# Kernel optimization log

Measured on AMD Instinct MI355X. Metric: run time of the kernel, lower is better.

The kernel has to match this reference:

```python
import jax, jax.numpy as jnp
import numpy as np

N = 50000      # nodes
E = 800000     # edges (before self-loops)
IN = 64        # input feature dim
SLOPE = 0.2    # leaky_relu negative slope
# layer specs: (heads, out_channels, concat)
LAYERS = [(8, 8, True), (8, 8, True), (4, 1, False)]


def _glorot(key, shape):
    fan = shape[-2] + shape[-1]
    lim = np.sqrt(6.0 / fan).astype(np.float32)
    return jax.random.uniform(key, shape, jnp.float32, -lim, lim)


def setup_inputs() -> dict:
    key = jax.random.key(0)
    ks = jax.random.split(key, 12)
    X = jax.random.normal(ks[0], (N, IN), jnp.float32)
    src = jax.random.randint(ks[1], (E,), 0, N)
    dst = jax.random.randint(ks[2], (E,), 0, N)
    dst = jnp.where(dst == src, (dst + 1) % N, dst)  # no self-loops (module removes then re-adds them)
    edge_index = jnp.stack([src, dst]).astype(jnp.int64)
    inp = {"X": X, "edge_index": edge_index}
    in_c = IN
    for li, (H, C, concat) in enumerate(LAYERS):
        k1, k2 = jax.random.split(ks[3 + li], 2)
        inp[f"W{li+1}"] = _glorot(k1, (in_c, H * C))
        inp[f"att{li+1}"] = _glorot(k2, (1, H, 2 * C))
        inp[f"b{li+1}"] = jnp.zeros((H * C if concat else C,), jnp.float32)
        in_c = H * C
    return inp


def _gat_layer(x, src, dst, W, att, b, heads, C, concat):
    # linear projection then view as [N, H, C]
    xw = (x @ W).reshape(-1, heads, C)
    # attention logits decompose: (cat[x_i, x_j] * att).sum(-1) = a_i[dst] + a_j[src]
    a_i = jnp.einsum('nhc,hc->nh', xw, att[0, :, :C])   # target-side score per node
    a_j = jnp.einsum('nhc,hc->nh', xw, att[0, :, C:])   # source-side score per node
    e = a_i[dst] + a_j[src]                              # [E', H]
    e = jnp.where(e > 0, e, SLOPE * e)                   # leaky_relu
    # segment softmax over edges sharing the same target node (stable)
    emax = jax.ops.segment_max(e, dst, num_segments=N)
    ex = jnp.exp(e - emax[dst])
    denom = jax.ops.segment_sum(ex, dst, num_segments=N)
    alpha = ex / denom[dst]                              # [E', H]
    # weighted scatter-add of source messages
    out = jax.ops.segment_sum(xw[src] * alpha[:, :, None], dst, num_segments=N)  # [N, H, C]
    out = out.reshape(-1, heads * C) if concat else out.mean(axis=1)
    return out + b


def reference(X, edge_index, W1, att1, b1, W2, att2, b2, W3, att3, b3):
    # add self-loops (module removes any existing then adds one per node)
    loop = jnp.arange(N, dtype=edge_index.dtype)
    src = jnp.concatenate([edge_index[0], loop])
    dst = jnp.concatenate([edge_index[1], loop])
    params = [(W1, att1, b1), (W2, att2, b2), (W3, att3, b3)]
    x = X
    for li, ((H, C, concat), (W, att, b)) in enumerate(zip(LAYERS, params)):
        x = _gat_layer(x, src, dst, W, att, b, H, C, concat)
        if li + 1 < len(LAYERS):
            x = jax.nn.relu(x)
    return x  # [N, 1]
```

## Files before the change

kernel.cpp:

```cpp
#include <hip/hip_runtime.h>
#include <hip/hip_bf16.h>
#include <hip/hip_fp16.h>
#include <float.h>


#define FDIM 64
#define BSHIFT 7
#define BNODES (1 << BSHIFT)
#define BINCH 8192

__device__ __forceinline__ int clampN(int v, int N) {
  return ((unsigned)v >= (unsigned)N) ? 0 : v;
}

__global__ __launch_bounds__(256) void init_kernel(
    const int* __restrict__ ei, int E, int* __restrict__ bucketCount, int NB,
    int* __restrict__ flag) {
  int i = blockIdx.x * 256 + threadIdx.x;
  if (i < NB) bucketCount[i] = 0;
  if (blockIdx.x == 0) {
    __shared__ int any;
    if (threadIdx.x == 0) any = 0;
    __syncthreads();
    int idx = 2 * threadIdx.x + 1;
    int v = (idx < 2 * E) ? ei[idx] : 0;
    if (v != 0) atomicOr(&any, 1);
    __syncthreads();
    if (threadIdx.x == 0) *flag = any ? 1 : 2;
  }
}

__global__ __launch_bounds__(256) void hist_kernel(
    const int* __restrict__ ei, const int* __restrict__ flag, int E, int N,
    int NB, int* __restrict__ bucketCount) {
  __shared__ int hist[512];
  int st = *flag;
  for (int i = threadIdx.x; i < NB; i += 256) hist[i] = 0;
  __syncthreads();
  int ET = E + N;
  for (int e = blockIdx.x * 256 + threadIdx.x; e < ET; e += gridDim.x * 256) {
    int dst = (e < E) ? clampN(ei[(size_t)st * (E + e)], N) : (e - E);
    atomicAdd(&hist[dst >> BSHIFT], 1);
  }
  __syncthreads();
  for (int i = threadIdx.x; i < NB; i += 256)
    if (hist[i]) atomicAdd(&bucketCount[i], hist[i]);
}

__global__ __launch_bounds__(512) void bucket_scan_kernel(
    const int* __restrict__ bucketCount, int NB, int* __restrict__ bucketBase,
    int* __restrict__ bucketFill, int* __restrict__ rowstart, int N, int ET) {
  __shared__ int s[512];
  int t = threadIdx.x;
  int v = (t < NB) ? bucketCount[t] : 0;
  s[t] = v;
  __syncthreads();
  for (int off = 1; off < 512; off <<= 1) {
    int x = (t >= off) ? s[t - off] : 0;
    __syncthreads();
    s[t] += x;
    __syncthreads();
  }
  if (t < NB) {
    int excl = s[t] - v;
    bucketBase[t] = excl;
    bucketFill[t] = excl;
  }
  if (t == 0) {
    bucketBase[NB] = s[511];
    rowstart[N] = ET;
  }
}

__global__ __launch_bounds__(256) void binscatter_kernel(
    const int* __restrict__ ei, const int* __restrict__ flag, int E, int N,
    int NB, int* __restrict__ bucketFill, unsigned* __restrict__ pairbuf,
    int ET) {
  __shared__ int hist[512];
  __shared__ int cursor[512];
  int st = *flag;
  int e0 = blockIdx.x * BINCH;
  int e1 = min(e0 + BINCH, ET);
  for (int i = threadIdx.x; i < NB; i += 256) hist[i] = 0;
  __syncthreads();
  for (int e = e0 + threadIdx.x; e < e1; e += 256) {
    int dst = (e < E) ? clampN(ei[(size_t)st * (E + e)], N) : (e - E);
    atomicAdd(&hist[dst >> BSHIFT], 1);
  }
  __syncthreads();
  for (int i = threadIdx.x; i < NB; i += 256)
    cursor[i] = hist[i] ? atomicAdd(&bucketFill[i], hist[i]) : 0;
  __syncthreads();
  for (int e = e0 + threadIdx.x; e < e1; e += 256) {
    int src, dst;
    if (e < E) {
      src = clampN(ei[(size_t)st * e], N);
      dst = clampN(ei[(size_t)st * (E + e)], N);
    } else {
      src = e - E; dst = e - E;
    }
    int pos = atomicAdd(&cursor[dst >> BSHIFT], 1);
    if ((unsigned)pos < (unsigned)ET)
      pairbuf[pos] = ((unsigned)src << BSHIFT) | (unsigned)(dst & (BNODES - 1));
  }
}

__global__ __launch_bounds__(256) void bucketbuild_kernel(
    const unsigned* __restrict__ pairbuf, const int* __restrict__ bucketBase,
    int N, int ET, int* __restrict__ rowstart, int* __restrict__ col) {
  __shared__ int s[BNODES];
  int b = blockIdx.x;
  int t = threadIdx.x;
  int base = bucketBase[b], end = bucketBase[b + 1];
  int n0 = b << BSHIFT;
  int nn = min(BNODES, N - n0);
  if (t < BNODES) s[t] = 0;
  __syncthreads();
  for (int e = base + t; e < end; e += 256) {
    int li = pairbuf[e] & (BNODES - 1);
    atomicAdd(&s[li], 1);
  }
  __syncthreads();
  int myd = (t < BNODES) ? s[t] : 0;
  for (int off = 1; off < BNODES; off <<= 1) {
    int v = (t >= off && t < BNODES) ? s[t - off] : 0;
    __syncthreads();
    if (t < BNODES) s[t] += v;
    __syncthreads();
  }
  int excl = (t < BNODES) ? (s[t] - myd) : 0;
  if (t < nn) rowstart[n0 + t] = base + excl;
  __syncthreads();
  if (t < BNODES) s[t] = excl;
  __syncthreads();
  for (int e = base + t; e < end; e += 256) {
    unsigned p = pairbuf[e];
    int li = p & (BNODES - 1);
    int pos = base + atomicAdd(&s[li], 1);
    if ((unsigned)pos < (unsigned)ET) col[pos] = (int)(p >> BSHIFT);
  }
}

__global__ __launch_bounds__(256) void gemm_att64_kernel(
    const float* __restrict__ x, const float* __restrict__ W,
    const float* __restrict__ att, int N, __half* __restrict__ xwh,
    float* __restrict__ ai, float* __restrict__ aj) {
  __shared__ float Wl[64 * 64];
  __shared__ float xqT[64 * 68];
  int tid = threadIdx.x;
  for (int i = tid; i < 64 * 64; i += 256) Wl[i] = W[i];
  int jq = tid & 15, nq = tid >> 4;
  float aI[4], aJ[4];
  #pragma unroll
  for (int ji = 0; ji < 4; ++ji) {
    int j = jq * 4 + ji, h = j >> 3, c = j & 7;
    aI[ji] = att[h * 16 + c];
    aJ[ji] = att[h * 16 + 8 + c];
  }
  int ntiles = (N + 63) >> 6;
  for (int tile = blockIdx.x; tile < ntiles; tile += gridDim.x) {
    int n0 = tile << 6;
    __syncthreads();
    for (int idx = tid; idx < 4096; idx += 256) {
      int n = idx >> 6, k = idx & 63;
      int gn = n0 + n;
      xqT[k * 68 + n] = (gn < N) ? x[(size_t)gn * 64 + k] : 0.f;
    }
    __syncthreads();
    float acc[4][4];
    #pragma unroll
    for (int i = 0; i < 4; ++i)
      #pragma unroll
      for (int j = 0; j < 4; ++j) acc[i][j] = 0.f;
    #pragma unroll 8
    for (int k = 0; k < 64; ++k) {
      float4 xv = *(const float4*)&xqT[k * 68 + nq * 4];
      float4 wv = *(const float4*)&Wl[k * 64 + jq * 4];
      acc[0][0] += xv.x * wv.x; acc[0][1] += xv.x * wv.y;
      acc[0][2] += xv.x * wv.z; acc[0][3] += xv.x * wv.w;
      acc[1][0] += xv.y * wv.x; acc[1][1] += xv.y * wv.y;
      acc[1][2] += xv.y * wv.z; acc[1][3] += xv.y * wv.w;
      acc[2][0] += xv.z * wv.x; acc[2][1] += xv.z * wv.y;
      acc[2][2] += xv.z * wv.z; acc[2][3] += xv.z * wv.w;
      acc[3][0] += xv.w * wv.x; acc[3][1] += xv.w * wv.y;
      acc[3][2] += xv.w * wv.z; acc[3][3] += xv.w * wv.w;
    }
    #pragma unroll
    for (int ni = 0; ni < 4; ++ni) {
      int gn = n0 + nq * 4 + ni;
      float pi = acc[ni][0] * aI[0] + acc[ni][1] * aI[1] +
                 acc[ni][2] * aI[2] + acc[ni][3] * aI[3];
      float pj = acc[ni][0] * aJ[0] + acc[ni][1] * aJ[1] +
                 acc[ni][2] * aJ[2] + acc[ni][3] * aJ[3];
      pi += __shfl_xor(pi, 1, 16);
      pj += __shfl_xor(pj, 1, 16);
      if (gn < N) {
        __half2 pk[2];
        pk[0] = __floats2half2_rn(acc[ni][0], acc[ni][1]);
        pk[1] = __floats2half2_rn(acc[ni][2], acc[ni][3]);
        *(uint2*)&xwh[(size_t)gn * 64 + jq * 4] = *(uint2*)pk;
        if (!(jq & 1)) {
          int h = jq >> 1;
          ai[gn * 8 + h] = pi;
          aj[gn * 8 + h] = pj;
        }
      }
    }
  }
}

__global__ __launch_bounds__(256) void gather64_kernel(
    const __half* __restrict__ xwh, const float* __restrict__ ai,
    const float* __restrict__ aj, const int* __restrict__ rowstart,
    const int* __restrict__ col, const float* __restrict__ bias, int N,
    float* __restrict__ out, int fuse3, const float* __restrict__ W3,
    const float* __restrict__ att3, float* __restrict__ pk3,
    float* __restrict__ ai3) {
  int n = blockIdx.x * 4 + (threadIdx.x >> 6);
  if (n >= N) return;
  int lane = threadIdx.x & 63;
  int slot = lane >> 4;
  int li = lane & 15;
  int f4 = li * 4;
  int h = li >> 1;
  int r0 = rowstart[n], r1 = rowstart[n + 1];
  float ain = ai[n * 8 + h];
  float dn = 0.f;
  float4 acc = make_float4(0.f, 0.f, 0.f, 0.f);
  int e = r0 + slot;
  for (; e + 12 < r1; e += 16) {
    int sA = clampN(col[e],      N);
    int sB = clampN(col[e + 4],  N);
    int sC = clampN(col[e + 8],  N);
    int sD = clampN(col[e + 12], N);
    float aA = aj[sA * 8 + h], aB = aj[sB * 8 + h];
    float aC = aj[sC * 8 + h], aD = aj[sD * 8 + h];
    uint2 rA = *(const uint2*)&xwh[(size_t)sA * 64 + f4];
    uint2 rB = *(const uint2*)&xwh[(size_t)sB * 64 + f4];
    uint2 rC = *(const uint2*)&xwh[(size_t)sC * 64 + f4];
    uint2 rD = *(const uint2*)&xwh[(size_t)sD * 64 + f4];
    float eA = ain + aA; eA = (eA > 0.f) ? eA : 0.2f * eA;
    float eB = ain + aB; eB = (eB > 0.f) ? eB : 0.2f * eB;
    float eC = ain + aC; eC = (eC > 0.f) ? eC : 0.2f * eC;
    float eD = ain + aD; eD = (eD > 0.f) ? eD : 0.2f * eD;
    float pA = __expf(eA), pB = __expf(eB);
    float pC = __expf(eC), pD = __expf(eD);
    dn += (pA + pB) + (pC + pD);
    float2 A0 = __half22float2(*(__half2*)&rA.x), A1 = __half22float2(*(__half2*)&rA.y);
    float2 B0 = __half22float2(*(__half2*)&rB.x), B1 = __half22float2(*(__half2*)&rB.y);
    float2 C0 = __half22float2(*(__half2*)&rC.x), C1 = __half22float2(*(__half2*)&rC.y);
    float2 D0 = __half22float2(*(__half2*)&rD.x), D1 = __half22float2(*(__half2*)&rD.y);
    acc.x += pA * A0.x + pB * B0.x + pC * C0.x + pD * D0.x;
    acc.y += pA * A0.y + pB * B0.y + pC * C0.y + pD * D0.y;
    acc.z += pA * A1.x + pB * B1.x + pC * C1.x + pD * D1.x;
    acc.w += pA * A1.y + pB * B1.y + pC * C1.y + pD * D1.y;
  }
  for (; e < r1; e += 4) {
    int s = clampN(col[e], N);
    float a = aj[s * 8 + h];
    uint2 r = *(const uint2*)&xwh[(size_t)s * 64 + f4];
    float ev = ain + a; ev = (ev > 0.f) ? ev : 0.2f * ev;
    float p = __expf(ev);
    dn += p;
    float2 v0 = __half22float2(*(__half2*)&r.x);
    float2 v1 = __half22float2(*(__half2*)&r.y);
    acc.x += p * v0.x; acc.y += p * v0.y;
    acc.z += p * v1.x; acc.w += p * v1.y;
  }
  dn += __shfl_xor(dn, 16); dn += __shfl_xor(dn, 32);
  acc.x += __shfl_xor(acc.x, 16); acc.x += __shfl_xor(acc.x, 32);
  acc.y += __shfl_xor(acc.y, 16); acc.y += __shfl_xor(acc.y, 32);
  acc.z += __shfl_xor(acc.z, 16); acc.z += __shfl_xor(acc.z, 32);
  acc.w += __shfl_xor(acc.w, 16); acc.w += __shfl_xor(acc.w, 32);
  float4 bv = *(const float4*)&bias[f4];
  float inv = 1.f / dn;
  float4 o = make_float4(fmaxf(acc.x * inv + bv.x, 0.f),
                         fmaxf(acc.y * inv + bv.y, 0.f),
                         fmaxf(acc.z * inv + bv.z, 0.f),
                         fmaxf(acc.w * inv + bv.w, 0.f));
  if (!fuse3) {
    if (slot == 0) *(float4*)&out[(size_t)n * 64 + f4] = o;
    return;
  }
  float4 w0 = *(const float4*)&W3[(f4 + 0) * 4];
  float4 w1 = *(const float4*)&W3[(f4 + 1) * 4];
  float4 w2 = *(const float4*)&W3[(f4 + 2) * 4];
  float4 w3 = *(const float4*)&W3[(f4 + 3) * 4];
  float pa0 = o.x * w0.x + o.y * w1.x + o.z * w2.x + o.w * w3.x;
  float pa1 = o.x * w0.y + o.y * w1.y + o.z * w2.y + o.w * w3.y;
  float pa2 = o.x * w0.z + o.y * w1.z + o.z * w2.z + o.w * w3.z;
  float pa3 = o.x * w0.w + o.y * w1.w + o.z * w2.w + o.w * w3.w;
  #pragma unroll
  for (int off = 1; off < 16; off <<= 1) {
    pa0 += __shfl_xor(pa0, off, 16);
    pa1 += __shfl_xor(pa1, off, 16);
    pa2 += __shfl_xor(pa2, off, 16);
    pa3 += __shfl_xor(pa3, off, 16);
  }
  if (lane == 0) {
    float a0 = att3[0], a1 = att3[1], a2 = att3[2], a3 = att3[3];
    float a4 = att3[4], a5 = att3[5], a6 = att3[6], a7 = att3[7];
    *(float4*)&pk3[(size_t)n * 8 + 0] = make_float4(pa0, pa0 * a1, pa1, pa1 * a3);
    *(float4*)&pk3[(size_t)n * 8 + 4] = make_float4(pa2, pa2 * a5, pa3, pa3 * a7);
    *(float4*)&ai3[(size_t)n * 4] = make_float4(pa0 * a0, pa1 * a2, pa2 * a4, pa3 * a6);
  }
}

__global__ __launch_bounds__(256) void gather4_kernel(
    const float* __restrict__ pk3, const float* __restrict__ ai3,
    const int* __restrict__ rowstart, const int* __restrict__ col,
    const float* __restrict__ b3, int N, float* __restrict__ out) {
  int t = blockIdx.x * 256 + threadIdx.x;
  int n = t >> 2;
  if (n >= N) return;
  int h = t & 3;
  int r0 = rowstart[n], r1 = rowstart[n + 1];
  float ain = ai3[n * 4 + h];
  float denom = 0.f, acc = 0.f;
  int e = r0;
  for (; e + 4 <= r1; e += 4) {
    int s0 = clampN(col[e + 0], N);
    int s1 = clampN(col[e + 1], N);
    int s2 = clampN(col[e + 2], N);
    int s3 = clampN(col[e + 3], N);
    float2 v0 = *(const float2*)&pk3[(size_t)s0 * 8 + h * 2];
    float2 v1 = *(const float2*)&pk3[(size_t)s1 * 8 + h * 2];
    float2 v2 = *(const float2*)&pk3[(size_t)s2 * 8 + h * 2];
    float2 v3 = *(const float2*)&pk3[(size_t)s3 * 8 + h * 2];
    float e0 = ain + v0.y; e0 = (e0 > 0.f) ? e0 : 0.2f * e0;
    float e1 = ain + v1.y; e1 = (e1 > 0.f) ? e1 : 0.2f * e1;
    float e2 = ain + v2.y; e2 = (e2 > 0.f) ? e2 : 0.2f * e2;
    float e3 = ain + v3.y; e3 = (e3 > 0.f) ? e3 : 0.2f * e3;
    float p0 = __expf(e0), p1 = __expf(e1);
    float p2 = __expf(e2), p3 = __expf(e3);
    denom += (p0 + p1) + (p2 + p3);
    acc += p0 * v0.x; acc += p1 * v1.x; acc += p2 * v2.x; acc += p3 * v3.x;
  }
  for (; e < r1; ++e) {
    int s = clampN(col[e], N);
    float2 v = *(const float2*)&pk3[(size_t)s * 8 + h * 2];
    float ev = ain + v.y;
    ev = (ev > 0.f) ? ev : 0.2f * ev;
    float p = __expf(ev);
    denom += p;
    acc += p * v.x;
  }
  float o = acc / denom;
  o += __shfl_xor(o, 1, 4);
  o += __shfl_xor(o, 2, 4);
  o *= 0.25f;
  if (h == 0) out[n] = o + b3[0];
}

extern "C" void kernel_launch(void* const* d_in, const int* in_sizes, int n_in,
                              void* d_out, int out_size, void* d_ws, size_t ws_size,
                              hipStream_t stream) {
  const float* X    = (const float*)d_in[0];
  const int*   ei   = (const int*)d_in[1];
  const float* W1   = (const float*)d_in[2];
  const float* att1 = (const float*)d_in[3];
  const float* b1   = (const float*)d_in[4];
  const float* W2   = (const float*)d_in[5];
  const float* att2 = (const float*)d_in[6];
  const float* b2   = (const float*)d_in[7];
  const float* W3   = (const float*)d_in[8];
  const float* att3 = (const float*)d_in[9];
  const float* b3   = (const float*)d_in[10];
  float* out = (float*)d_out;

  const int N  = in_sizes[0] / FDIM;
  const int E  = in_sizes[1] / 2;
  const int ET = E + N;
  const int NB = (N + BNODES - 1) >> BSHIFT;

  char* ws = (char*)d_ws;
  auto carve = [&](size_t bytes) {
    char* p = ws; ws += (bytes + 15) & ~(size_t)15; return p;
  };
  __half*   xwh       = (__half*)carve((size_t)N * 64 * 2);
  float*    hfeat     = (float*)carve((size_t)N * 64 * 4);
  float*    pk3       = (float*)carve((size_t)N * 8 * 4);
  float*    ai3       = (float*)carve((size_t)N * 4 * 4);
  float*    ai        = (float*)carve((size_t)N * 8 * 4);
  float*    aj        = (float*)carve((size_t)N * 8 * 4);
  int*      rowstart  = (int*)carve((size_t)(N + 1) * 4);
  int*      colidx    = (int*)carve((size_t)ET * 4);
  int*      stflag    = (int*)carve(16);
  int*      bucketCnt = (int*)carve(512 * 4);
  int*      bucketBas = (int*)carve(513 * 4);
  int*      bucketFil = (int*)carve(512 * 4);
  size_t need = (size_t)(ws - (char*)d_ws);
  if (ws_size < need) return;
  unsigned* pairbuf = (unsigned*)hfeat;

  init_kernel<<<(NB + 255) / 256 + 1, 256, 0, stream>>>(ei, E, bucketCnt, NB, stflag);
  hist_kernel<<<128, 256, 0, stream>>>(ei, stflag, E, N, NB, bucketCnt);
  bucket_scan_kernel<<<1, 512, 0, stream>>>(bucketCnt, NB, bucketBas, bucketFil,
                                            rowstart, N, ET);
  binscatter_kernel<<<(ET + BINCH - 1) / BINCH, 256, 0, stream>>>(
      ei, stflag, E, N, NB, bucketFil, pairbuf, ET);
  bucketbuild_kernel<<<NB, 256, 0, stream>>>(pairbuf, bucketBas, N, ET,
                                             rowstart, colidx);

  const int nodeBlocks4 = (N + 3) / 4;
  const int laneBlocks4 = (N * 4 + 255) / 256;
  const int gemmTiles   = (N + 63) / 64;

  gemm_att64_kernel<<<gemmTiles, 256, 0, stream>>>(X, W1, att1, N, xwh, ai, aj);
  gather64_kernel<<<nodeBlocks4, 256, 0, stream>>>(
      xwh, ai, aj, rowstart, colidx, b1, N, hfeat, 0, nullptr, nullptr,
      nullptr, nullptr);
  gemm_att64_kernel<<<gemmTiles, 256, 0, stream>>>(hfeat, W2, att2, N, xwh, ai, aj);
  gather64_kernel<<<nodeBlocks4, 256, 0, stream>>>(
      xwh, ai, aj, rowstart, colidx, b2, N, nullptr, 1, W3, att3, pk3, ai3);
  gather4_kernel<<<laneBlocks4, 256, 0, stream>>>(pk3, ai3, rowstart, colidx,
                                                  b3, N, out);
}
```

Baseline: 242.4 us.

## Split gather64 feature columns across two blocks and unfuse layer-3 projection

The 64-wide gather kernel now assigns each node's feature vector to two blocks, each handling 32 columns with 8 edge slots per wavefront instead of 4. This doubles the number of blocks and the edge-level parallelism per node, at the cost of reading column indices and attention scores twice. The layer-3 projection that was fused into the second gather moves into a separate small GEMM kernel, which adds a launch and a round trip of the 64-wide hidden features through memory.

Measured after the change: 267.1 us. 1.1x slower.

```diff
diff --git a/kernel.cpp b/kernel.cpp
--- a/kernel.cpp
+++ b/kernel.cpp
@@ -209,53 +209,61 @@
   }
 }
 
+__global__ __launch_bounds__(256) void gemm_att4_kernel(
+    const float* __restrict__ x, const float* __restrict__ W,
+    const float* __restrict__ att, int N, float* __restrict__ pk3,
+    float* __restrict__ ai3) {
+  int t = blockIdx.x * 256 + threadIdx.x;
+  int n = t >> 2;
+  if (n >= N) return;
+  int j = t & 3;
+  const float* xr = x + (size_t)n * 64;
+  float acc = 0.f;
+  #pragma unroll
+  for (int k = 0; k < 64; ++k) acc += xr[k] * W[k * 4 + j];
+  pk3[(size_t)n * 8 + j * 2]     = acc;
+  pk3[(size_t)n * 8 + j * 2 + 1] = acc * att[j * 2 + 1];
+  ai3[(size_t)n * 4 + j]         = acc * att[j * 2];
+}
+
 __global__ __launch_bounds__(256) void gather64_kernel(
     const __half* __restrict__ xwh, const float* __restrict__ ai,
     const float* __restrict__ aj, const int* __restrict__ rowstart,
     const int* __restrict__ col, const float* __restrict__ bias, int N,
-    float* __restrict__ out, int fuse3, const float* __restrict__ W3,
-    const float* __restrict__ att3, float* __restrict__ pk3,
-    float* __restrict__ ai3) {
-  int n = blockIdx.x * 4 + (threadIdx.x >> 6);
+    float* __restrict__ out) {
+  int bid = blockIdx.x;
+  int half = (bid >> 2) & 1;
+  int quad = (bid >> 3) * 4 + (bid & 3);
+  int n = quad * 4 + (threadIdx.x >> 6);
   if (n >= N) return;
   int lane = threadIdx.x & 63;
-  int slot = lane >> 4;
-  int li = lane & 15;
-  int f4 = li * 4;
-  int h = li >> 1;
+  int slot = lane >> 3;
+  int li = lane & 7;
+  int f4 = half * 32 + li * 4;
+  int h = f4 >> 3;
   int r0 = rowstart[n], r1 = rowstart[n + 1];
   float ain = ai[n * 8 + h];
   float dn = 0.f;
   float4 acc = make_float4(0.f, 0.f, 0.f, 0.f);
   int e = r0 + slot;
-  for (; e + 12 < r1; e += 16) {
-    int sA = clampN(col[e],      N);
-    int sB = clampN(col[e + 4],  N);
-    int sC = clampN(col[e + 8],  N);
-    int sD = clampN(col[e + 12], N);
+  for (; e + 8 < r1; e += 16) {
+    int sA = clampN(col[e],     N);
+    int sB = clampN(col[e + 8], N);
     float aA = aj[sA * 8 + h], aB = aj[sB * 8 + h];
-    float aC = aj[sC * 8 + h], aD = aj[sD * 8 + h];
     uint2 rA = *(const uint2*)&xwh[(size_t)sA * 64 + f4];
     uint2 rB = *(const uint2*)&xwh[(size_t)sB * 64 + f4];
-    uint2 rC = *(const uint2*)&xwh[(size_t)sC * 64 + f4];
-    uint2 rD = *(const uint2*)&xwh[(size_t)sD * 64 + f4];
     float eA = ain + aA; eA = (eA > 0.f) ? eA : 0.2f * eA;
     float eB = ain + aB; eB = (eB > 0.f) ? eB : 0.2f * eB;
-    float eC = ain + aC; eC = (eC > 0.f) ? eC : 0.2f * eC;
-    float eD = ain + aD; eD = (eD > 0.f) ? eD : 0.2f * eD;
     float pA = __expf(eA), pB = __expf(eB);
-    float pC = __expf(eC), pD = __expf(eD);
-    dn += (pA + pB) + (pC + pD);
+    dn += pA + pB;
     float2 A0 = __half22float2(*(__half2*)&rA.x), A1 = __half22float2(*(__half2*)&rA.y);
     float2 B0 = __half22float2(*(__half2*)&rB.x), B1 = __half22float2(*(__half2*)&rB.y);
-    float2 C0 = __half22float2(*(__half2*)&rC.x), C1 = __half22float2(*(__half2*)&rC.y);
-    float2 D0 = __half22float2(*(__half2*)&rD.x), D1 = __half22float2(*(__half2*)&rD.y);
-    acc.x += pA * A0.x + pB * B0.x + pC * C0.x + pD * D0.x;
-    acc.y += pA * A0.y + pB * B0.y + pC * C0.y + pD * D0.y;
-    acc.z += pA * A1.x + pB * B1.x + pC * C1.x + pD * D1.x;
-    acc.w += pA * A1.y + pB * B1.y + pC * C1.y + pD * D1.y;
-  }
-  for (; e < r1; e += 4) {
+    acc.x += pA * A0.x + pB * B0.x;
+    acc.y += pA * A0.y + pB * B0.y;
+    acc.z += pA * A1.x + pB * B1.x;
+    acc.w += pA * A1.y + pB * B1.y;
+  }
+  if (e < r1) {
     int s = clampN(col[e], N);
     float a = aj[s * 8 + h];
     uint2 r = *(const uint2*)&xwh[(size_t)s * 64 + f4];
@@ -267,42 +275,19 @@
     acc.x += p * v0.x; acc.y += p * v0.y;
     acc.z += p * v1.x; acc.w += p * v1.y;
   }
-  dn += __shfl_xor(dn, 16); dn += __shfl_xor(dn, 32);
-  acc.x += __shfl_xor(acc.x, 16); acc.x += __shfl_xor(acc.x, 32);
-  acc.y += __shfl_xor(acc.y, 16); acc.y += __shfl_xor(acc.y, 32);
-  acc.z += __shfl_xor(acc.z, 16); acc.z += __shfl_xor(acc.z, 32);
-  acc.w += __shfl_xor(acc.w, 16); acc.w += __shfl_xor(acc.w, 32);
-  float4 bv = *(const float4*)&bias[f4];
-  float inv = 1.f / dn;
-  float4 o = make_float4(fmaxf(acc.x * inv + bv.x, 0.f),
-                         fmaxf(acc.y * inv + bv.y, 0.f),
-                         fmaxf(acc.z * inv + bv.z, 0.f),
-                         fmaxf(acc.w * inv + bv.w, 0.f));
-  if (!fuse3) {
-    if (slot == 0) *(float4*)&out[(size_t)n * 64 + f4] = o;
-    return;
-  }
-  float4 w0 = *(const float4*)&W3[(f4 + 0) * 4];
-  float4 w1 = *(const float4*)&W3[(f4 + 1) * 4];
-  float4 w2 = *(const float4*)&W3[(f4 + 2) * 4];
-  float4 w3 = *(const float4*)&W3[(f4 + 3) * 4];
-  float pa0 = o.x * w0.x + o.y * w1.x + o.z * w2.x + o.w * w3.x;
-  float pa1 = o.x * w0.y + o.y * w1.y + o.z * w2.y + o.w * w3.y;
-  float pa2 = o.x * w0.z + o.y * w1.z + o.z * w2.z + o.w * w3.z;
-  float pa3 = o.x * w0.w + o.y * w1.w + o.z * w2.w + o.w * w3.w;
-  #pragma unroll
-  for (int off = 1; off < 16; off <<= 1) {
-    pa0 += __shfl_xor(pa0, off, 16);
-    pa1 += __shfl_xor(pa1, off, 16);
-    pa2 += __shfl_xor(pa2, off, 16);
-    pa3 += __shfl_xor(pa3, off, 16);
-  }
-  if (lane == 0) {
-    float a0 = att3[0], a1 = att3[1], a2 = att3[2], a3 = att3[3];
-    float a4 = att3[4], a5 = att3[5], a6 = att3[6], a7 = att3[7];
-    *(float4*)&pk3[(size_t)n * 8 + 0] = make_float4(pa0, pa0 * a1, pa1, pa1 * a3);
-    *(float4*)&pk3[(size_t)n * 8 + 4] = make_float4(pa2, pa2 * a5, pa3, pa3 * a7);
-    *(float4*)&ai3[(size_t)n * 4] = make_float4(pa0 * a0, pa1 * a2, pa2 * a4, pa3 * a6);
+  dn += __shfl_xor(dn, 8); dn += __shfl_xor(dn, 16); dn += __shfl_xor(dn, 32);
+  acc.x += __shfl_xor(acc.x, 8); acc.x += __shfl_xor(acc.x, 16); acc.x += __shfl_xor(acc.x, 32);
+  acc.y += __shfl_xor(acc.y, 8); acc.y += __shfl_xor(acc.y, 16); acc.y += __shfl_xor(acc.y, 32);
+  acc.z += __shfl_xor(acc.z, 8); acc.z += __shfl_xor(acc.z, 16); acc.z += __shfl_xor(acc.z, 32);
+  acc.w += __shfl_xor(acc.w, 8); acc.w += __shfl_xor(acc.w, 16); acc.w += __shfl_xor(acc.w, 32);
+  if (slot == 0) {
+    float4 bv = *(const float4*)&bias[f4];
+    float inv = 1.f / dn;
+    float4 o = make_float4(fmaxf(acc.x * inv + bv.x, 0.f),
+                           fmaxf(acc.y * inv + bv.y, 0.f),
+                           fmaxf(acc.z * inv + bv.z, 0.f),
+                           fmaxf(acc.w * inv + bv.w, 0.f));
+    *(float4*)&out[(size_t)n * 64 + f4] = o;
   }
 }
 
@@ -402,17 +387,18 @@
   bucketbuild_kernel<<<NB, 256, 0, stream>>>(pairbuf, bucketBas, N, ET,
                                              rowstart, colidx);
 
-  const int nodeBlocks4 = (N + 3) / 4;
+  const int nquads      = (N + 3) / 4;
+  const int gatherGrid  = ((nquads + 3) / 4) * 8;
   const int laneBlocks4 = (N * 4 + 255) / 256;
   const int gemmTiles   = (N + 63) / 64;
 
   gemm_att64_kernel<<<gemmTiles, 256, 0, stream>>>(X, W1, att1, N, xwh, ai, aj);
-  gather64_kernel<<<nodeBlocks4, 256, 0, stream>>>(
-      xwh, ai, aj, rowstart, colidx, b1, N, hfeat, 0, nullptr, nullptr,
-      nullptr, nullptr);
+  gather64_kernel<<<gatherGrid, 256, 0, stream>>>(xwh, ai, aj, rowstart, colidx,
+                                                  b1, N, hfeat);
   gemm_att64_kernel<<<gemmTiles, 256, 0, stream>>>(hfeat, W2, att2, N, xwh, ai, aj);
-  gather64_kernel<<<nodeBlocks4, 256, 0, stream>>>(
-      xwh, ai, aj, rowstart, colidx, b2, N, nullptr, 1, W3, att3, pk3, ai3);
+  gather64_kernel<<<gatherGrid, 256, 0, stream>>>(xwh, ai, aj, rowstart, colidx,
+                                                  b2, N, hfeat);
+  gemm_att4_kernel<<<laneBlocks4, 256, 0, stream>>>(hfeat, W3, att3, N, pk3, ai3);
   gather4_kernel<<<laneBlocks4, 256, 0, stream>>>(pk3, ai3, rowstart, colidx,
                                                   b3, N, out);
 }
```
